# Optimization experiments

Measured on AMD Instinct MI355X. Metric: run time of the kernel, lower is better.

## Reference

```python
import jax, jax.numpy as jnp
import numpy as np


def setup_inputs() -> dict:
    key = jax.random.key(0)
    k1, k2 = jax.random.split(key)
    x = jax.random.normal(k1, (4, 2048, 512), dtype=jnp.float32)
    proxy = jax.random.normal(k2, (16, 512), dtype=jnp.float32)
    return {"x": x, "proxy": proxy}


def reference(x, proxy):
    # x: (B, S, D), proxy: (P, D)
    num_proxies = proxy.shape[0]
    # prods: (B, P, S) = proxy @ x^T per batch
    prods = jnp.einsum('pd,bsd->bps', proxy, x)
    # broadcast outer product: (B, P, S, D), then running prefix sum over seq
    y = jnp.cumsum(prods[..., None] * x[:, None, :, :], axis=2)
    # softmax gate over proxies (dim=1), scaled by sqrt(P)
    w = jax.nn.softmax(prods / jnp.sqrt(jnp.float32(num_proxies)), axis=1)
    # weighted sum over proxies -> (B, S, D)
    out = jnp.einsum('bps,bpsd->bsd', w, y)
    return out
```

## Files before the change

### kernel.cpp

```cpp
#include <hip/hip_runtime.h>
#include <hip/hip_bf16.h>

#define B 4
#define S 2048
#define D 512
#define P 16
#define NC 64
#define CL 32

__global__ __launch_bounds__(256) void k_prods(const float* __restrict__ x,
                                               const float* __restrict__ proxy,
                                               float* __restrict__ prods,
                                               float* __restrict__ wgt) {
    const int wave = (blockIdx.x * blockDim.x + threadIdx.x) >> 6;
    const int lane = threadIdx.x & 63;
    const int bs0  = wave * 4;

    float4 pA[P], pB[P];
#pragma unroll
    for (int p = 0; p < P; ++p) {
        const float* pr = proxy + p * D + lane * 8;
        pA[p] = *(const float4*)pr;
        pB[p] = *(const float4*)(pr + 4);
    }

#pragma unroll
    for (int r = 0; r < 4; ++r) {
        const int bs = bs0 + r;
        const float* xr = x + (size_t)bs * D + lane * 8;
        float4 xa = *(const float4*)xr;
        float4 xb = *(const float4*)(xr + 4);

        float part[P];
#pragma unroll
        for (int p = 0; p < P; ++p) {
            part[p] = xa.x*pA[p].x + xa.y*pA[p].y + xa.z*pA[p].z + xa.w*pA[p].w
                    + xb.x*pB[p].x + xb.y*pB[p].y + xb.z*pB[p].z + xb.w*pB[p].w;
        }

        float a8[8];
#pragma unroll
        for (int k = 0; k < 8; ++k) {
            bool hi = lane & 1;
            float mine = hi ? part[2*k+1] : part[2*k];
            float oth  = hi ? part[2*k]   : part[2*k+1];
            a8[k] = mine + __shfl_xor(oth, 1);
        }
        float a4[4];
#pragma unroll
        for (int k = 0; k < 4; ++k) {
            bool hi = lane & 2;
            float mine = hi ? a8[2*k+1] : a8[2*k];
            float oth  = hi ? a8[2*k]   : a8[2*k+1];
            a4[k] = mine + __shfl_xor(oth, 2);
        }
        float a2[2];
#pragma unroll
        for (int k = 0; k < 2; ++k) {
            bool hi = lane & 4;
            float mine = hi ? a4[2*k+1] : a4[2*k];
            float oth  = hi ? a4[2*k]   : a4[2*k+1];
            a2[k] = mine + __shfl_xor(oth, 4);
        }
        float a1;
        {
            bool hi = lane & 8;
            float mine = hi ? a2[1] : a2[0];
            float oth  = hi ? a2[0] : a2[1];
            a1 = mine + __shfl_xor(oth, 8);
        }
        a1 += __shfl_xor(a1, 16);
        a1 += __shfl_xor(a1, 32);

        float m = a1;
#pragma unroll
        for (int off = 1; off < 16; off <<= 1) m = fmaxf(m, __shfl_xor(m, off));
        float e = __expf((a1 - m) * 0.25f);
        float den = e;
#pragma unroll
        for (int off = 1; off < 16; off <<= 1) den += __shfl_xor(den, off);

        if (lane < P) {
            prods[(size_t)bs * P + lane] = a1;
            wgt  [(size_t)bs * P + lane] = e / den;
        }
    }
}

__global__ __launch_bounds__(256) void k_totals(const float* __restrict__ x,
                                                const float* __restrict__ prods,
                                                float* __restrict__ T) {
    int h = blockIdx.x & 1;
    int c = (blockIdx.x >> 1) & (NC - 1);
    int b = blockIdx.x >> 7;
    int d = h * 256 + threadIdx.x;

    float acc[P];
#pragma unroll
    for (int p = 0; p < P; ++p) acc[p] = 0.f;

    int bs0 = b * S + c * CL;
#pragma unroll 4
    for (int i = 0; i < CL; ++i) {
        int bs = bs0 + i;
        float xv = x[(size_t)bs * D + d];
        const float4* pp = (const float4*)(prods + (size_t)bs * P);
        float pr[P];
        ((float4*)pr)[0] = pp[0];
        ((float4*)pr)[1] = pp[1];
        ((float4*)pr)[2] = pp[2];
        ((float4*)pr)[3] = pp[3];
#pragma unroll
        for (int p = 0; p < P; ++p) acc[p] = fmaf(pr[p], xv, acc[p]);
    }
    size_t tb = ((size_t)(b * NC + c)) * (P * D) + d;
#pragma unroll
    for (int p = 0; p < P; ++p) T[tb + p * D] = acc[p];
}

__global__ __launch_bounds__(256) void k_scan(float* __restrict__ T) {
    int t = blockIdx.x * blockDim.x + threadIdx.x;
    int d = t & (D - 1);
    int p = (t >> 9) & (P - 1);
    int b = t >> 13;
    size_t base = ((size_t)b * NC * P + p) * D + d;
    float run = 0.f;
#pragma unroll 8
    for (int c = 0; c < NC; ++c) {
        size_t idx = base + (size_t)c * (P * D);
        float v = T[idx];
        T[idx] = run;
        run += v;
    }
}

__global__ __launch_bounds__(256) void k_apply(const float* __restrict__ x,
                                               const float* __restrict__ prods,
                                               const float* __restrict__ wgt,
                                               const float* __restrict__ T,
                                               float* __restrict__ out) {
    int h = blockIdx.x & 1;
    int c = (blockIdx.x >> 1) & (NC - 1);
    int b = blockIdx.x >> 7;
    int d = h * 256 + threadIdx.x;

    float st[P];
    size_t tb = ((size_t)(b * NC + c)) * (P * D) + d;
#pragma unroll
    for (int p = 0; p < P; ++p) st[p] = T[tb + p * D];

    int bs0 = b * S + c * CL;
#pragma unroll 2
    for (int i = 0; i < CL; ++i) {
        int bs = bs0 + i;
        float xv = x[(size_t)bs * D + d];
        const float4* pp = (const float4*)(prods + (size_t)bs * P);
        const float4* wp = (const float4*)(wgt   + (size_t)bs * P);
        float pr[P], ww[P];
        ((float4*)pr)[0] = pp[0];
        ((float4*)pr)[1] = pp[1];
        ((float4*)pr)[2] = pp[2];
        ((float4*)pr)[3] = pp[3];
        ((float4*)ww)[0] = wp[0];
        ((float4*)ww)[1] = wp[1];
        ((float4*)ww)[2] = wp[2];
        ((float4*)ww)[3] = wp[3];
        float o = 0.f;
#pragma unroll
        for (int p = 0; p < P; ++p) {
            st[p] = fmaf(pr[p], xv, st[p]);
            o = fmaf(ww[p], st[p], o);
        }
        out[(size_t)bs * D + d] = o;
    }
}

extern "C" void kernel_launch(void* const* d_in, const int* in_sizes, int n_in,
                              void* d_out, int out_size, void* d_ws, size_t ws_size,
                              hipStream_t stream) {
    const float* x     = (const float*)d_in[0];
    const float* proxy = (const float*)d_in[1];
    float* out   = (float*)d_out;

    float* prods = (float*)d_ws;
    float* wgt   = prods + (size_t)B * S * P;
    float* T     = wgt   + (size_t)B * S * P;

    k_prods <<<(B * S) / 4 / 4,   256, 0, stream>>>(x, proxy, prods, wgt);
    k_totals<<<B * NC * 2,        256, 0, stream>>>(x, prods, T);
    k_scan  <<<(B * P * D) / 256, 256, 0, stream>>>(T);
    k_apply <<<B * NC * 2,        256, 0, stream>>>(x, prods, wgt, T, out);
}
```

Before: 36.13 us.

## Use finer sequence chunks and a two-level parallel chunk scan

The number of chunks doubles (NC 64→128, CL 32→16), which doubles the blocks in the totals and apply kernels to fill more CUs. The chunk-prefix scan becomes two-level: each block handles 64 d values of one (b,p), and four waves each scan 32 chunks in registers, then combine their totals through shared memory. This shortens the serial chain in k_scan, at the cost of a larger T buffer (twice the traffic) and a 32-float register array per thread.

```diff
diff --git a/kernel.cpp b/kernel.cpp
--- a/kernel.cpp
+++ b/kernel.cpp
@@ -5,8 +5,8 @@
 #define S 2048
 #define D 512
 #define P 16
-#define NC 64
-#define CL 32
+#define NC 128
+#define CL 16
 
 __global__ __launch_bounds__(256) void k_prods(const float* __restrict__ x,
                                                const float* __restrict__ proxy,
@@ -92,7 +92,7 @@
                                                 float* __restrict__ T) {
     int h = blockIdx.x & 1;
     int c = (blockIdx.x >> 1) & (NC - 1);
-    int b = blockIdx.x >> 7;
+    int b = blockIdx.x >> 8;
     int d = h * 256 + threadIdx.x;
 
     float acc[P];
@@ -119,18 +119,38 @@
 }
 
 __global__ __launch_bounds__(256) void k_scan(float* __restrict__ T) {
-    int t = blockIdx.x * blockDim.x + threadIdx.x;
-    int d = t & (D - 1);
-    int p = (t >> 9) & (P - 1);
-    int b = t >> 13;
-    size_t base = ((size_t)b * NC * P + p) * D + d;
+    __shared__ float s_tot[4][64];
+
+    const int dgrp = blockIdx.x & 7;
+    const int p    = (blockIdx.x >> 3) & 15;
+    const int b    = blockIdx.x >> 7;
+    const int dl   = threadIdx.x & 63;
+    const int g    = threadIdx.x >> 6;
+    const int d    = dgrp * 64 + dl;
+
+    const size_t chunk_stride = (size_t)P * D;
+    const size_t base = ((size_t)b * NC * P + p) * D + d + (size_t)(g * 32) * chunk_stride;
+
+    float v[32];
+#pragma unroll 8
+    for (int c = 0; c < 32; ++c) v[c] = T[base + (size_t)c * chunk_stride];
+
+    float tot = 0.f;
+#pragma unroll
+    for (int c = 0; c < 32; ++c) tot += v[c];
+
+    s_tot[g][dl] = tot;
+    __syncthreads();
+
     float run = 0.f;
-#pragma unroll 8
-    for (int c = 0; c < NC; ++c) {
-        size_t idx = base + (size_t)c * (P * D);
-        float v = T[idx];
-        T[idx] = run;
-        run += v;
+#pragma unroll
+    for (int gg = 0; gg < 3; ++gg)
+        if (gg < g) run += s_tot[gg][dl];
+
+    #pragma unroll 8
+    for (int c = 0; c < 32; ++c) {
+        T[base + (size_t)c * chunk_stride] = run;
+        run += v[c];
     }
 }
 
@@ -141,7 +161,7 @@
                                                float* __restrict__ out) {
     int h = blockIdx.x & 1;
     int c = (blockIdx.x >> 1) & (NC - 1);
-    int b = blockIdx.x >> 7;
+    int b = blockIdx.x >> 8;
     int d = h * 256 + threadIdx.x;
 
     float st[P];
@@ -186,8 +206,8 @@
     float* wgt   = prods + (size_t)B * S * P;
     float* T     = wgt   + (size_t)B * S * P;
 
-    k_prods <<<(B * S) / 4 / 4,   256, 0, stream>>>(x, proxy, prods, wgt);
-    k_totals<<<B * NC * 2,        256, 0, stream>>>(x, prods, T);
-    k_scan  <<<(B * P * D) / 256, 256, 0, stream>>>(T);
-    k_apply <<<B * NC * 2,        256, 0, stream>>>(x, prods, wgt, T, out);
-}
+    k_prods <<<(B * S) / 16,  256, 0, stream>>>(x, proxy, prods, wgt);
+    k_totals<<<B * NC * 2,    256, 0, stream>>>(x, prods, T);
+    k_scan  <<<B * P * 8,     256, 0, stream>>>(T);
+    k_apply <<<B * NC * 2,    256, 0, stream>>>(x, prods, wgt, T, out);
+}
```

New measurement: 44.15 us. 1.22x slower.
